# Kernel tuning notes

Measured on AMD Instinct MI355X. Metric: run time of the kernel, lower is better.

## Reference

```python
import jax, jax.numpy as jnp
import numpy as np
from jax import lax

SQRT2 = 1.4142135623730951
SCALE_BOUND = 0.11
LIK_BOUND = 1e-9

def conv2d(x, w, b, pad):
    y = lax.conv_general_dilated(x, w, (1, 1), [(pad, pad), (pad, pad)],
                                 dimension_numbers=('NCHW', 'OIHW', 'NCHW'))
    return y + b[None, :, None, None]

def space_to_depth(x):  # pixel_unshuffle, block=2: [B,C,H,W]->[B,4C,H/2,W/2]
    B, C, H, W = x.shape
    x = x.reshape(B, C, H // 2, 2, W // 2, 2)
    return x.transpose(0, 1, 3, 5, 2, 4).reshape(B, 4 * C, H // 2, W // 2)

def lrelu(x):
    return jnp.where(x >= 0, x, 0.01 * x)

def gauss_cdf(x):
    return 0.5 * (1.0 + lax.erf(x / SQRT2))

def setup_inputs() -> dict:
    key = jax.random.key(0)
    ks = jax.random.split(key, 6)
    B, F_, P, H, W = 4, 128, 128, 256, 256
    inp = {
        'input': jax.random.normal(ks[0], (B, F_, H, W), jnp.float32) * 2.0,
        'condition': jax.random.normal(ks[1], (B, P // 4, H, W), jnp.float32),
        'lstm_w': jax.random.normal(ks[2], (4 * P, F_ + P, 3, 3), jnp.float32) * 0.02,
        'lstm_b': jnp.zeros((4 * P,), jnp.float32),
        'w1': jax.random.normal(ks[3], (2 * F_, P + F_, 1, 1), jnp.float32) * 0.05,
        'b1': jnp.zeros((2 * F_,), jnp.float32),
        'w2': jax.random.normal(ks[4], (2 * F_, 2 * F_, 3, 3), jnp.float32) * 0.02,
        'b2': jnp.zeros((2 * F_,), jnp.float32),
        'w3': jax.random.normal(ks[5], (2 * F_, 2 * F_, 1, 1), jnp.float32) * 0.05,
        'b3': jnp.zeros((2 * F_,), jnp.float32),
    }
    return inp

def reference(input, condition, lstm_w, lstm_b, w1, b1, w2, b2, w3, b3):
    # quantize (round with straight-through estimator, as in trc quant)
    q = input + lax.stop_gradient(jnp.round(input) - input)
    y = space_to_depth(q)                       # [B,4F,h,w]
    groups = jnp.split(y, 4, axis=1)
    if condition.shape[-2:] == input.shape[-2:]:
        condition = space_to_depth(condition)   # [B,P,h,w]
    h = condition
    c = condition
    lls = []
    for g in range(4):
        yi = groups[g - 1] if g else jnp.zeros_like(groups[0])
        # ConvLSTM cell: single conv over [input, hidden] -> 4 gates
        gates = conv2d(jnp.concatenate([yi, h], axis=1), lstm_w, lstm_b, 1)
        i_g, f_g, o_g, g_g = jnp.split(gates, 4, axis=1)
        c = jax.nn.sigmoid(f_g) * c + jax.nn.sigmoid(i_g) * jnp.tanh(g_g)
        h = jax.nn.sigmoid(o_g) * jnp.tanh(c)
        # reparam stack -> (mean, scale) condition
        t = lrelu(conv2d(jnp.concatenate([h, yi], axis=1), w1, b1, 0))
        t = lrelu(conv2d(t, w2, b2, 1))
        cnd = conv2d(t, w3, b3, 0)
        mean, scale = jnp.split(cnd, 2, axis=1)
        scale = jnp.maximum(scale, SCALE_BOUND)
        z = groups[g]
        up = gauss_cdf((z - mean + 0.5) / scale)
        lo = gauss_cdf((z - mean - 0.5) / scale)
        lls.append(jnp.maximum(up - lo, LIK_BOUND))
    likelihood = jnp.concatenate(lls, axis=1)   # [B,4F,h,w]
    return q, likelihood
```

## Files before the change

kernel.cpp:

```cpp
#include <hip/hip_runtime.h>
#include <math.h>

typedef unsigned short u16;
typedef __attribute__((ext_vector_type(8))) short bf16x8;
typedef __attribute__((ext_vector_type(4))) float f32x4;

#define PSUB 2163200
#define TSUB 2097152

__device__ __forceinline__ u16 f2bf(float f) {
  unsigned u = __float_as_uint(f);
  unsigned r = u + 0x7fffu + ((u >> 16) & 1u);
  return (u16)(r >> 16);
}
__device__ __forceinline__ float bf2f(u16 h) {
  return __uint_as_float(((unsigned)h) << 16);
}
__device__ __forceinline__ void gl16(const u16* g, const u16* l) {
  __builtin_amdgcn_global_load_lds(
      (const __attribute__((address_space(1))) void*)g,
      (__attribute__((address_space(3))) void*)l, 16, 0, 0);
}

__global__ void quant_s2d_kernel(const float* __restrict__ inp,
                                 float* __restrict__ q,
                                 u16* __restrict__ yghi) {
  int idx = blockIdx.x * 256 + threadIdx.x;
  int ww = idx & 255;
  int hh = (idx >> 8) & 255;
  int cc = (idx >> 16) & 127;
  int b  = idx >> 23;
  float v = rintf(inp[idx]);
  q[idx] = v;
  int g = cc >> 5;
  int f = ((cc & 31) << 2) | ((hh & 1) << 1) | (ww & 1);
  int y = hh >> 1, x = ww >> 1;
  int p = (b * 130 + y + 1) * 130 + 1 + x;
  yghi[(size_t)g * 4 * PSUB + (size_t)(f >> 5) * PSUB + (size_t)p * 32 + (f & 31)] = f2bf(v);
}

__global__ void s2d_cond_kernel(const float* __restrict__ cond,
                                u16* __restrict__ hhi, float* __restrict__ c0) {
  int idx = blockIdx.x * 256 + threadIdx.x;
  int ww = idx & 255;
  int hh = (idx >> 8) & 255;
  int cc = (idx >> 16) & 31;
  int b  = idx >> 21;
  float v = cond[idx];
  int ch = (cc << 2) | ((hh & 1) << 1) | (ww & 1);
  int y = hh >> 1, x = ww >> 1;
  int p = (b * 130 + y + 1) * 130 + 1 + x;
  hhi[(size_t)(ch >> 5) * PSUB + (size_t)p * 32 + (ch & 31)] = f2bf(v);
  c0[((size_t)(b * 128 + y) * 128 + x) * 128 + ch] = v;
}

template <int TAPS, int PERM>
__global__ void build_wpack(const float* __restrict__ w, u16* __restrict__ o) {
  int idx = blockIdx.x * 256 + threadIdx.x;
  int jj = idx & 7, lane = (idx >> 3) & 63, ni = (idx >> 9) & 3, wn = (idx >> 11) & 1;
  int rest = idx >> 12;
  const int NSLAB = TAPS * 8;
  int slab = rest % NSLAB, cb = rest / NSLAB;
  int c = cb * 128 + wn * 64 + ni * 16 + (lane & 15);
  int k = slab * 32 + ((lane >> 4) << 3) + jj;
  int tap = (TAPS == 9) ? (k >> 8) : 0;
  int ci = (TAPS == 9) ? (k & 255) : k;
  int oc;
  if (PERM == 0)      oc = ((c >> 4) & 3) * 128 + (c >> 7) * 32 + ((c >> 6) & 1) * 16 + (c & 15);
  else if (PERM == 2) oc = ((c >> 4) & 1) * 128 + (c >> 7) * 64 + ((c >> 6) & 1) * 32 + ((c >> 5) & 1) * 16 + (c & 15);
  else                oc = c;
  float v = w[((size_t)(oc * 256 + ci)) * TAPS + tap];
  o[idx] = f2bf(v);
}

__global__ void make_biases(const float* __restrict__ lb, const float* __restrict__ b1,
                            const float* __restrict__ b2, const float* __restrict__ b3,
                            float* __restrict__ pl, float* __restrict__ p1,
                            float* __restrict__ p2, float* __restrict__ p3) {
  int t = blockIdx.x * 256 + threadIdx.x;
  if (t < 512) {
    int gate = (t >> 4) & 3;
    int f = (t >> 7) * 32 + ((t >> 6) & 1) * 16 + (t & 15);
    pl[t] = lb[gate * 128 + f];
  }
  if (t < 256) {
    p1[t] = b1[t];
    p2[t] = b2[t];
    int m = (t >> 4) & 1;
    int f = (t >> 7) * 64 + ((t >> 6) & 1) * 32 + ((t >> 5) & 1) * 16 + (t & 15);
    p3[t] = b3[m * 128 + f];
  }
}

template <int TAPS, int NCOL, int EPI>
__global__ __launch_bounds__(256, 4)
void conv_mfma(const u16* __restrict__ a0, const u16* __restrict__ a1,
               int RS, int PAD, int skiphalf,
               const u16* __restrict__ Wpk, const float* __restrict__ biasP,
               float* __restrict__ c_io,
               u16* __restrict__ ohi, size_t OSUB, int ORS, int OPAD,
               const u16* __restrict__ zsrc, float* __restrict__ lik, int g) {
  constexpr int NSLAB = TAPS * 8;
  constexpr int NCB = NCOL / 128;
  __shared__ __attribute__((aligned(16))) u16 lds[16384];
  const int tid = threadIdx.x;
  const int lane = tid & 63, wid = tid >> 6;
  const int wm = wid >> 1, wn = wid & 1;
  const int fl = lane & 15, kq = lane >> 4;

  int n = blockIdx.y * NCB + blockIdx.x;
  int w_ = n >> 9, r_ = n & 511;
  int xj = r_ & 7, tt = r_ >> 3;
  const int cb = tt & (NCB - 1);
  const int YL = 64 / NCB;
  int ystrip = w_ * (8 * YL) + xj * YL + (tt / NCB);
  const int b = ystrip >> 7, y = ystrip & 127;

  const int NS = skiphalf ? NSLAB / 2 : NSLAB;
  f32x4 acc[4][4] = {};

  auto mapslab = [&](int si) -> int {
    if (!skiphalf) return si;
    int tap = si >> 2, o = si & 3;
    return tap * 8 + (skiphalf == 1 ? 4 + o : o);
  };
  auto stage = [&](int si, int buf) {
    int s = mapslab(si);
    int dy = 0, dx = 0;
    if (TAPS == 9) { int tap = s >> 3; dy = tap / 3 - 1; dx = tap % 3 - 1; }
    int cc = s & 7;
    const u16* ap = ((cc < 4) ? a0 : a1) + (size_t)(cc & 3) * ((TAPS == 1 && EPI == 2) ? (size_t)TSUB : (size_t)PSUB);
    int origin = (b * RS + y + PAD) * RS + PAD + dy * RS + dx;
    const u16* abase = ap + (size_t)origin * 32;
    const u16* wbase = Wpk + ((size_t)(cb * NSLAB + s)) * 4096;
#pragma unroll
    for (int t = 0; t < 2; ++t) {
      int j = wid * 2 + t;
      gl16(abase + j * 512 + lane * 8, &lds[buf * 4096 + j * 512]);
    }
#pragma unroll
    for (int t = 0; t < 2; ++t) {
      int j = wid * 2 + t;
      gl16(wbase + j * 512 + lane * 8, &lds[8192 + buf * 4096 + j * 512]);
    }
  };
  auto compute = [&](int buf) {
    bf16x8 Ah[4], Wf[4];
#pragma unroll
    for (int i = 0; i < 4; ++i)
      Ah[i] = *(const bf16x8*)&lds[buf * 4096 + (wm * 64 + i * 16 + fl) * 32 + kq * 8];
#pragma unroll
    for (int i = 0; i < 4; ++i)
      Wf[i] = *(const bf16x8*)&lds[8192 + buf * 4096 + wn * 2048 + i * 512 + lane * 8];
    __builtin_amdgcn_s_setprio(1);
#pragma unroll
    for (int mi = 0; mi < 4; ++mi)
#pragma unroll
      for (int ni = 0; ni < 4; ++ni)
        acc[mi][ni] = __builtin_amdgcn_mfma_f32_16x16x32_bf16(Ah[mi], Wf[ni], acc[mi][ni], 0, 0, 0);
    __builtin_amdgcn_s_setprio(0);
  };

  stage(0, 0);
  for (int s = 0; s < NS; ++s) {
    if (s + 1 < NS) {
      stage(s + 1, (s + 1) & 1);
      asm volatile("s_waitcnt vmcnt(4)" ::: "memory");
    } else {
      asm volatile("s_waitcnt vmcnt(0)" ::: "memory");
    }
    __builtin_amdgcn_s_barrier();
    compute(s & 1);
    __builtin_amdgcn_s_barrier();
  }

  if (EPI == 0) {
    const int f = cb * 32 + wn * 16 + fl;
    float bi[4];
#pragma unroll
    for (int ni = 0; ni < 4; ++ni) bi[ni] = biasP[cb * 128 + wn * 64 + ni * 16 + fl];
#pragma unroll
    for (int mi = 0; mi < 4; ++mi)
#pragma unroll
      for (int r = 0; r < 4; ++r) {
        int x = wm * 64 + mi * 16 + kq * 4 + r;
        size_t ci = ((size_t)(b * 128 + y) * 128 + x) * 128 + f;
        float ig = 1.f / (1.f + expf(-(acc[mi][0][r] + bi[0])));
        float fg = 1.f / (1.f + expf(-(acc[mi][1][r] + bi[1])));
        float og = 1.f / (1.f + expf(-(acc[mi][2][r] + bi[2])));
        float gg = tanhf(acc[mi][3][r] + bi[3]);
        float cn = fg * c_io[ci] + ig * gg;
        c_io[ci] = cn;
        float hv = og * tanhf(cn);
        size_t hx = (size_t)((b * 130 + y + 1) * 130 + 1 + x);
        ohi[(size_t)(f >> 5) * PSUB + hx * 32 + (f & 31)] = f2bf(hv);
      }
  } else if (EPI == 1) {
#pragma unroll
    for (int ni = 0; ni < 4; ++ni) {
      int c = cb * 128 + wn * 64 + ni * 16 + fl;
      float bv = biasP[c];
#pragma unroll
      for (int mi = 0; mi < 4; ++mi)
#pragma unroll
        for (int r = 0; r < 4; ++r) {
          int x = wm * 64 + mi * 16 + kq * 4 + r;
          float v = acc[mi][ni][r] + bv;
          v = (v >= 0.f) ? v : 0.01f * v;
          size_t op = (size_t)((b * ORS + y + OPAD) * ORS + OPAD + x);
          ohi[(size_t)(c >> 5) * OSUB + op * 32 + (c & 31)] = f2bf(v);
        }
    }
  } else {
#pragma unroll
    for (int j = 0; j < 2; ++j) {
      int f = cb * 64 + wn * 32 + j * 16 + fl;
      float bm = biasP[cb * 128 + wn * 64 + j * 32 + fl];
      float bs = biasP[cb * 128 + wn * 64 + j * 32 + 16 + fl];
#pragma unroll
      for (int mi = 0; mi < 4; ++mi)
#pragma unroll
        for (int r = 0; r < 4; ++r) {
          int x = wm * 64 + mi * 16 + kq * 4 + r;
          float mean = acc[mi][2 * j][r] + bm;
          float sc = fmaxf(acc[mi][2 * j + 1][r] + bs, 0.11f);
          size_t zp = (size_t)((b * 130 + y + 1) * 130 + 1 + x);
          float z = bf2f(zsrc[(size_t)(f >> 5) * PSUB + zp * 32 + (f & 31)]);
          float is = 0.70710678118654752f / sc;
          float up = 0.5f * (1.f + erff((z - mean + 0.5f) * is));
          float lo_ = 0.5f * (1.f + erff((z - mean - 0.5f) * is));
          lik[((size_t)(b * 512 + g * 128 + f) * 128 + y) * 128 + x] = fmaxf(up - lo_, 1e-9f);
        }
    }
  }
}

extern "C" void kernel_launch(void* const* d_in, const int* in_sizes, int n_in,
                              void* d_out, int out_size, void* d_ws, size_t ws_size,
                              hipStream_t stream) {
  const float* input  = (const float*)d_in[0];
  const float* cond   = (const float*)d_in[1];
  const float* lstm_w = (const float*)d_in[2];
  const float* lstm_b = (const float*)d_in[3];
  const float* w1 = (const float*)d_in[4];
  const float* b1 = (const float*)d_in[5];
  const float* w2 = (const float*)d_in[6];
  const float* b2 = (const float*)d_in[7];
  const float* w3 = (const float*)d_in[8];
  const float* b3 = (const float*)d_in[9];

  float* q   = (float*)d_out;
  float* lik = q + 33554432;

  char* ws = (char*)d_ws;
  u16* YG    = (u16*)(ws + 0);
  u16* HAhi  = (u16*)(ws + 69222400);
  u16* HBhi  = (u16*)(ws + 86528000);
  u16* T1hi  = (u16*)(ws + 103833600);
  u16* T2hi  = (u16*)(ws + 138444800);
  float* cbuf = (float*)(ws + 171999232);
  u16* WLpk = (u16*)(ws + 205553664);
  u16* W2pk = (u16*)(ws + 207912960);
  u16* W1pk = (u16*)(ws + 209092608);
  u16* W3pk = (u16*)(ws + 209223680);
  float* PL = (float*)(ws + 209354752);
  float* P1 = PL + 512;
  float* P2 = P1 + 256;
  float* P3 = P2 + 256;

  hipMemsetAsync(ws, 0, 138444800, stream);

  quant_s2d_kernel<<<131072, 256, 0, stream>>>(input, q, YG);
  s2d_cond_kernel<<<32768, 256, 0, stream>>>(cond, HAhi, cbuf);
  build_wpack<9, 0><<<4608, 256, 0, stream>>>(lstm_w, WLpk);
  build_wpack<9, 1><<<2304, 256, 0, stream>>>(w2, W2pk);
  build_wpack<1, 1><<<256, 256, 0, stream>>>(w1, W1pk);
  build_wpack<1, 2><<<256, 256, 0, stream>>>(w3, W3pk);
  make_biases<<<2, 256, 0, stream>>>(lstm_b, b1, b2, b3, PL, P1, P2, P3);

  for (int g = 0; g < 4; ++g) {
    u16* hinhi  = (g & 1) ? HBhi : HAhi;
    u16* houthi = (g & 1) ? HAhi : HBhi;
    const u16* yihi = g ? (YG + (size_t)(g - 1) * 4 * PSUB) : hinhi;
    const u16* zg = YG + (size_t)g * 4 * PSUB;

    conv_mfma<9, 512, 0><<<dim3(4, 512), 256, 0, stream>>>(
        yihi, hinhi, 130, 1, g ? 0 : 1,
        WLpk, PL, cbuf, houthi, PSUB, 0, 0, nullptr, nullptr, g);
    conv_mfma<1, 256, 1><<<dim3(2, 512), 256, 0, stream>>>(
        houthi, yihi, 130, 1, g ? 0 : 2,
        W1pk, P1, nullptr, T1hi, PSUB, 130, 1, nullptr, nullptr, g);
    conv_mfma<9, 256, 1><<<dim3(2, 512), 256, 0, stream>>>(
        T1hi, T1hi + (size_t)4 * PSUB, 130, 1, 0,
        W2pk, P2, nullptr, T2hi, TSUB, 128, 0, nullptr, nullptr, g);
    conv_mfma<1, 256, 2><<<dim3(2, 512), 256, 0, stream>>>(
        T2hi, T2hi + (size_t)4 * TSUB, 128, 0, 0,
        W3pk, P3, nullptr, nullptr, 0, 0, 0, zg, lik, g);
  }
}
```

Measured before the change: 1.341 ms.

## Widen conv tiles to 128x256 and switch activations to 8-channel subplanes

Each block now computes all 128 pixels of a row against 256 output columns, with four waves split only along N, so every wave reuses A fragments across eight M tiles. Activations move from 32-channel interleaved planes to 8-channel planes so A loads stay contiguous under the new LDS layout. Weight slabs double in size, LDS grows, accumulators double, and launch bounds drop to 2 blocks per CU. This cuts A re-reads and halves the grid at the cost of occupancy and register pressure.

Result: slower. 1.392 ms (+3.8%).

```diff
diff --git a/kernel.cpp b/kernel.cpp
--- a/kernel.cpp
+++ b/kernel.cpp
@@ -5,8 +5,8 @@
 typedef __attribute__((ext_vector_type(8))) short bf16x8;
 typedef __attribute__((ext_vector_type(4))) float f32x4;
 
-#define PSUB 2163200
-#define TSUB 2097152
+#define PSUB8 540800
+#define TSUB8 524288
 
 __device__ __forceinline__ u16 f2bf(float f) {
   unsigned u = __float_as_uint(f);
@@ -36,7 +36,7 @@
   int f = ((cc & 31) << 2) | ((hh & 1) << 1) | (ww & 1);
   int y = hh >> 1, x = ww >> 1;
   int p = (b * 130 + y + 1) * 130 + 1 + x;
-  yghi[(size_t)g * 4 * PSUB + (size_t)(f >> 5) * PSUB + (size_t)p * 32 + (f & 31)] = f2bf(v);
+  yghi[((size_t)(g * 16 + (f >> 3))) * PSUB8 + (size_t)p * 8 + (f & 7)] = f2bf(v);
 }
 
 __global__ void s2d_cond_kernel(const float* __restrict__ cond,
@@ -50,18 +50,18 @@
   int ch = (cc << 2) | ((hh & 1) << 1) | (ww & 1);
   int y = hh >> 1, x = ww >> 1;
   int p = (b * 130 + y + 1) * 130 + 1 + x;
-  hhi[(size_t)(ch >> 5) * PSUB + (size_t)p * 32 + (ch & 31)] = f2bf(v);
+  hhi[(size_t)(ch >> 3) * PSUB8 + (size_t)p * 8 + (ch & 7)] = f2bf(v);
   c0[((size_t)(b * 128 + y) * 128 + x) * 128 + ch] = v;
 }
 
 template <int TAPS, int PERM>
 __global__ void build_wpack(const float* __restrict__ w, u16* __restrict__ o) {
   int idx = blockIdx.x * 256 + threadIdx.x;
-  int jj = idx & 7, lane = (idx >> 3) & 63, ni = (idx >> 9) & 3, wn = (idx >> 11) & 1;
-  int rest = idx >> 12;
+  int jj = idx & 7, lane = (idx >> 3) & 63, ni = (idx >> 9) & 3, wn = (idx >> 11) & 3;
+  int rest = idx >> 13;
   const int NSLAB = TAPS * 8;
   int slab = rest % NSLAB, cb = rest / NSLAB;
-  int c = cb * 128 + wn * 64 + ni * 16 + (lane & 15);
+  int c = cb * 256 + wn * 64 + ni * 16 + (lane & 15);
   int k = slab * 32 + ((lane >> 4) << 3) + jj;
   int tap = (TAPS == 9) ? (k >> 8) : 0;
   int ci = (TAPS == 9) ? (k & 255) : k;
@@ -93,7 +93,7 @@
 }
 
 template <int TAPS, int NCOL, int EPI>
-__global__ __launch_bounds__(256, 4)
+__global__ __launch_bounds__(256, 2)
 void conv_mfma(const u16* __restrict__ a0, const u16* __restrict__ a1,
                int RS, int PAD, int skiphalf,
                const u16* __restrict__ Wpk, const float* __restrict__ biasP,
@@ -101,11 +101,11 @@
                u16* __restrict__ ohi, size_t OSUB, int ORS, int OPAD,
                const u16* __restrict__ zsrc, float* __restrict__ lik, int g) {
   constexpr int NSLAB = TAPS * 8;
-  constexpr int NCB = NCOL / 128;
-  __shared__ __attribute__((aligned(16))) u16 lds[16384];
+  constexpr int NCB = NCOL / 256;
+  constexpr size_t PST = (TAPS == 1 && EPI == 2) ? (size_t)TSUB8 : (size_t)PSUB8;
+  __shared__ __attribute__((aligned(16))) u16 lds[24576];
   const int tid = threadIdx.x;
-  const int lane = tid & 63, wid = tid >> 6;
-  const int wm = wid >> 1, wn = wid & 1;
+  const int lane = tid & 63, wn = tid >> 6;
   const int fl = lane & 15, kq = lane >> 4;
 
   int n = blockIdx.y * NCB + blockIdx.x;
@@ -117,7 +117,7 @@
   const int b = ystrip >> 7, y = ystrip & 127;
 
   const int NS = skiphalf ? NSLAB / 2 : NSLAB;
-  f32x4 acc[4][4] = {};
+  f32x4 acc[8][4] = {};
 
   auto mapslab = [&](int si) -> int {
     if (!skiphalf) return si;
@@ -129,35 +129,35 @@
     int dy = 0, dx = 0;
     if (TAPS == 9) { int tap = s >> 3; dy = tap / 3 - 1; dx = tap % 3 - 1; }
     int cc = s & 7;
-    const u16* ap = ((cc < 4) ? a0 : a1) + (size_t)(cc & 3) * ((TAPS == 1 && EPI == 2) ? (size_t)TSUB : (size_t)PSUB);
+    const u16* base = (cc < 4) ? a0 : a1;
     int origin = (b * RS + y + PAD) * RS + PAD + dy * RS + dx;
-    const u16* abase = ap + (size_t)origin * 32;
-    const u16* wbase = Wpk + ((size_t)(cb * NSLAB + s)) * 4096;
 #pragma unroll
     for (int t = 0; t < 2; ++t) {
-      int j = wid * 2 + t;
-      gl16(abase + j * 512 + lane * 8, &lds[buf * 4096 + j * 512]);
-    }
-#pragma unroll
-    for (int t = 0; t < 2; ++t) {
-      int j = wid * 2 + t;
-      gl16(wbase + j * 512 + lane * 8, &lds[8192 + buf * 4096 + j * 512]);
+      int j = wn * 2 + t;
+      const u16* src = base + (size_t)((cc & 3) * 4 + (j >> 1)) * PST
+                            + (size_t)(origin + (j & 1) * 64) * 8;
+      gl16(src + lane * 8, &lds[buf * 4096 + j * 512]);
+    }
+    const u16* wbase = Wpk + ((size_t)(cb * NSLAB + s)) * 8192;
+#pragma unroll
+    for (int t = 0; t < 4; ++t) {
+      int j = wn * 4 + t;
+      gl16(wbase + j * 512 + lane * 8, &lds[8192 + buf * 8192 + j * 512]);
     }
   };
   auto compute = [&](int buf) {
-    bf16x8 Ah[4], Wf[4];
+    bf16x8 Wf[4];
 #pragma unroll
     for (int i = 0; i < 4; ++i)
-      Ah[i] = *(const bf16x8*)&lds[buf * 4096 + (wm * 64 + i * 16 + fl) * 32 + kq * 8];
-#pragma unroll
-    for (int i = 0; i < 4; ++i)
-      Wf[i] = *(const bf16x8*)&lds[8192 + buf * 4096 + wn * 2048 + i * 512 + lane * 8];
+      Wf[i] = *(const bf16x8*)&lds[8192 + buf * 8192 + wn * 2048 + i * 512 + lane * 8];
     __builtin_amdgcn_s_setprio(1);
 #pragma unroll
-    for (int mi = 0; mi < 4; ++mi)
+    for (int mi = 0; mi < 8; ++mi) {
+      bf16x8 Ah = *(const bf16x8*)&lds[buf * 4096 + kq * 1024 + (mi * 16 + fl) * 8];
 #pragma unroll
       for (int ni = 0; ni < 4; ++ni)
-        acc[mi][ni] = __builtin_amdgcn_mfma_f32_16x16x32_bf16(Ah[mi], Wf[ni], acc[mi][ni], 0, 0, 0);
+        acc[mi][ni] = __builtin_amdgcn_mfma_f32_16x16x32_bf16(Ah, Wf[ni], acc[mi][ni], 0, 0, 0);
+    }
     __builtin_amdgcn_s_setprio(0);
   };
 
@@ -165,7 +165,7 @@
   for (int s = 0; s < NS; ++s) {
     if (s + 1 < NS) {
       stage(s + 1, (s + 1) & 1);
-      asm volatile("s_waitcnt vmcnt(4)" ::: "memory");
+      asm volatile("s_waitcnt vmcnt(6)" ::: "memory");
     } else {
       asm volatile("s_waitcnt vmcnt(0)" ::: "memory");
     }
@@ -175,15 +175,15 @@
   }
 
   if (EPI == 0) {
-    const int f = cb * 32 + wn * 16 + fl;
+    const int f = cb * 64 + wn * 16 + fl;
     float bi[4];
 #pragma unroll
-    for (int ni = 0; ni < 4; ++ni) bi[ni] = biasP[cb * 128 + wn * 64 + ni * 16 + fl];
-#pragma unroll
-    for (int mi = 0; mi < 4; ++mi)
+    for (int ni = 0; ni < 4; ++ni) bi[ni] = biasP[cb * 256 + wn * 64 + ni * 16 + fl];
+#pragma unroll
+    for (int mi = 0; mi < 8; ++mi)
 #pragma unroll
       for (int r = 0; r < 4; ++r) {
-        int x = wm * 64 + mi * 16 + kq * 4 + r;
+        int x = mi * 16 + kq * 4 + r;
         size_t ci = ((size_t)(b * 128 + y) * 128 + x) * 128 + f;
         float ig = 1.f / (1.f + expf(-(acc[mi][0][r] + bi[0])));
         float fg = 1.f / (1.f + expf(-(acc[mi][1][r] + bi[1])));
@@ -193,39 +193,39 @@
         c_io[ci] = cn;
         float hv = og * tanhf(cn);
         size_t hx = (size_t)((b * 130 + y + 1) * 130 + 1 + x);
-        ohi[(size_t)(f >> 5) * PSUB + hx * 32 + (f & 31)] = f2bf(hv);
+        ohi[(size_t)(f >> 3) * PSUB8 + hx * 8 + (f & 7)] = f2bf(hv);
       }
   } else if (EPI == 1) {
 #pragma unroll
     for (int ni = 0; ni < 4; ++ni) {
-      int c = cb * 128 + wn * 64 + ni * 16 + fl;
+      int c = wn * 64 + ni * 16 + fl;
       float bv = biasP[c];
 #pragma unroll
-      for (int mi = 0; mi < 4; ++mi)
+      for (int mi = 0; mi < 8; ++mi)
 #pragma unroll
         for (int r = 0; r < 4; ++r) {
-          int x = wm * 64 + mi * 16 + kq * 4 + r;
+          int x = mi * 16 + kq * 4 + r;
           float v = acc[mi][ni][r] + bv;
           v = (v >= 0.f) ? v : 0.01f * v;
           size_t op = (size_t)((b * ORS + y + OPAD) * ORS + OPAD + x);
-          ohi[(size_t)(c >> 5) * OSUB + op * 32 + (c & 31)] = f2bf(v);
+          ohi[(size_t)(c >> 3) * OSUB + op * 8 + (c & 7)] = f2bf(v);
         }
     }
   } else {
 #pragma unroll
     for (int j = 0; j < 2; ++j) {
-      int f = cb * 64 + wn * 32 + j * 16 + fl;
-      float bm = biasP[cb * 128 + wn * 64 + j * 32 + fl];
-      float bs = biasP[cb * 128 + wn * 64 + j * 32 + 16 + fl];
-#pragma unroll
-      for (int mi = 0; mi < 4; ++mi)
+      int f = wn * 32 + j * 16 + fl;
+      float bm = biasP[wn * 64 + j * 32 + fl];
+      float bs = biasP[wn * 64 + j * 32 + 16 + fl];
+#pragma unroll
+      for (int mi = 0; mi < 8; ++mi)
 #pragma unroll
         for (int r = 0; r < 4; ++r) {
-          int x = wm * 64 + mi * 16 + kq * 4 + r;
+          int x = mi * 16 + kq * 4 + r;
           float mean = acc[mi][2 * j][r] + bm;
           float sc = fmaxf(acc[mi][2 * j + 1][r] + bs, 0.11f);
           size_t zp = (size_t)((b * 130 + y + 1) * 130 + 1 + x);
-          float z = bf2f(zsrc[(size_t)(f >> 5) * PSUB + zp * 32 + (f & 31)]);
+          float z = bf2f(zsrc[(size_t)(f >> 3) * PSUB8 + zp * 8 + (f & 7)]);
           float is = 0.70710678118654752f / sc;
           float up = 0.5f * (1.f + erff((z - mean + 0.5f) * is));
           float lo_ = 0.5f * (1.f + erff((z - mean - 0.5f) * is));
@@ -281,20 +281,20 @@
   for (int g = 0; g < 4; ++g) {
     u16* hinhi  = (g & 1) ? HBhi : HAhi;
     u16* houthi = (g & 1) ? HAhi : HBhi;
-    const u16* yihi = g ? (YG + (size_t)(g - 1) * 4 * PSUB) : hinhi;
-    const u16* zg = YG + (size_t)g * 4 * PSUB;
-
-    conv_mfma<9, 512, 0><<<dim3(4, 512), 256, 0, stream>>>(
+    const u16* yihi = g ? (YG + (size_t)(g - 1) * 16 * PSUB8) : hinhi;
+    const u16* zg = YG + (size_t)g * 16 * PSUB8;
+
+    conv_mfma<9, 512, 0><<<dim3(2, 512), 256, 0, stream>>>(
         yihi, hinhi, 130, 1, g ? 0 : 1,
-        WLpk, PL, cbuf, houthi, PSUB, 0, 0, nullptr, nullptr, g);
-    conv_mfma<1, 256, 1><<<dim3(2, 512), 256, 0, stream>>>(
+        WLpk, PL, cbuf, houthi, PSUB8, 0, 0, nullptr, nullptr, g);
+    conv_mfma<1, 256, 1><<<dim3(1, 512), 256, 0, stream>>>(
         houthi, yihi, 130, 1, g ? 0 : 2,
-        W1pk, P1, nullptr, T1hi, PSUB, 130, 1, nullptr, nullptr, g);
-    conv_mfma<9, 256, 1><<<dim3(2, 512), 256, 0, stream>>>(
-        T1hi, T1hi + (size_t)4 * PSUB, 130, 1, 0,
-        W2pk, P2, nullptr, T2hi, TSUB, 128, 0, nullptr, nullptr, g);
-    conv_mfma<1, 256, 2><<<dim3(2, 512), 256, 0, stream>>>(
-        T2hi, T2hi + (size_t)4 * TSUB, 128, 0, 0,
+        W1pk, P1, nullptr, T1hi, PSUB8, 130, 1, nullptr, nullptr, g);
+    conv_mfma<9, 256, 1><<<dim3(1, 512), 256, 0, stream>>>(
+        T1hi, T1hi + (size_t)16 * PSUB8, 130, 1, 0,
+        W2pk, P2, nullptr, T2hi, TSUB8, 128, 0, nullptr, nullptr, g);
+    conv_mfma<1, 256, 2><<<dim3(1, 512), 256, 0, stream>>>(
+        T2hi, T2hi + (size_t)16 * TSUB8, 128, 0, 0,
         W3pk, P3, nullptr, nullptr, 0, 0, 0, zg, lik, g);
   }
 }
```
